# Kernel optimization log

Measured on AMD Instinct MI355X. Metric: run time of the kernel, lower is better.

The kernel has to match this reference:

```python
import jax, jax.numpy as jnp
import numpy as np

DIM = 1536
HEADS = 12
HD = DIM // HEADS  # 128
EPS = 1e-6
SINK_SIZE = 1          # frames
MAX_ATTN = 1920        # tokens (sliding window)


def setup_inputs() -> dict:
    key = jax.random.key(0)
    ks = jax.random.split(key, 10)
    B = 1
    F, H, W = 8, 16, 24
    L = F * H * W  # 3072
    s = 0.02
    inp = {
        "x": jax.random.normal(ks[0], (B, L, DIM), jnp.float32),
        "seq_lens": jnp.array([L], jnp.int32),
        "grid_sizes": jnp.array([[F, H, W]], jnp.int32),
        "freqs": jax.random.normal(ks[1], (1024, HD // 2, 2), jnp.float32),
        "wq": jax.random.normal(ks[2], (DIM, DIM), jnp.float32) * s,
        "bq": jnp.zeros((DIM,), jnp.float32),
        "wk": jax.random.normal(ks[3], (DIM, DIM), jnp.float32) * s,
        "bk": jnp.zeros((DIM,), jnp.float32),
        "wv": jax.random.normal(ks[4], (DIM, DIM), jnp.float32) * s,
        "bv": jnp.zeros((DIM,), jnp.float32),
        "wo": jax.random.normal(ks[5], (DIM, DIM), jnp.float32) * s,
        "bo": jnp.zeros((DIM,), jnp.float32),
        "nq_w": jnp.ones((DIM,), jnp.float32),
        "nk_w": jnp.ones((DIM,), jnp.float32),
    }
    return inp


def _rmsnorm(x, w):
    # WanRMSNorm: x * rsqrt(mean(x^2) + eps) * weight
    return x * jax.lax.rsqrt(jnp.mean(x * x, axis=-1, keepdims=True) + EPS) * w


def _rope(x, F, H, W, fc):
    # x: [B, L, n, d]; fc: complex [1024, d//2]
    B, L, n, d = x.shape
    c = d // 2
    c1 = c - 2 * (c // 3)  # temporal split
    c2 = c // 3
    f0, f1, f2 = fc[:, :c1], fc[:, c1:c1 + c2], fc[:, c1 + c2:]
    fr = jnp.concatenate([
        jnp.broadcast_to(f0[:F, None, None, :], (F, H, W, c1)),
        jnp.broadcast_to(f1[None, :H, None, :], (F, H, W, c2)),
        jnp.broadcast_to(f2[None, None, :W, :], (F, H, W, c2)),
    ], axis=-1).reshape(L, 1, c)  # [L, 1, c]
    xp = x.reshape(B, L, n, c, 2)
    xc = jax.lax.complex(xp[..., 0], xp[..., 1])  # [B, L, n, c]
    xr = xc * fr[None]
    return jnp.stack([jnp.real(xr), jnp.imag(xr)], axis=-1).reshape(B, L, n, d)


def reference(x, seq_lens, grid_sizes, freqs, wq, bq, wk, bk, wv, bv, wo, bo, nq_w, nk_w):
    B, L, _ = x.shape
    gs = np.asarray(grid_sizes)[0]
    F, H, W = int(gs[0]), int(gs[1]), int(gs[2])
    fs = H * W  # frame_seqlen
    sink = SINK_SIZE * fs

    q = _rmsnorm(x @ wq.T + bq, nq_w).reshape(B, L, HEADS, HD)
    k = _rmsnorm(x @ wk.T + bk, nk_w).reshape(B, L, HEADS, HD)
    v = (x @ wv.T + bv).reshape(B, L, HEADS, HD)

    fc = jax.lax.complex(freqs[..., 0], freqs[..., 1])  # [1024, HD//2]
    q = _rope(q, F, H, W, fc)
    k = _rope(k, F, H, W, fc)

    # sink + windowed frame-causal block mask (flex_attention block_mask)
    idx = jnp.arange(L)
    qf = idx // fs
    kf = idx // fs
    mask = (kf[None, :] <= qf[:, None]) & (
        (idx[None, :] < sink) | (idx[None, :] >= (qf[:, None] + 1) * fs - MAX_ATTN)
    )  # [L, L]

    scale = 1.0 / np.float32(np.sqrt(HD))
    scores = jnp.einsum('bqnd,bknd->bnqk', q, k) * scale
    scores = jnp.where(mask[None, None], scores, jnp.float32(-1e30))
    attn = jax.nn.softmax(scores, axis=-1)
    out = jnp.einsum('bnqk,bknd->bqnd', attn, v).reshape(B, L, DIM)
    return out @ wo.T + bo
```

## Files before the change

kernel.cpp:

```cpp
#include <hip/hip_runtime.h>
#include <stdint.h>

#define DIMC 1536
#define LTOK 3072
#define HEADS 12
#define HD 128
#define FS 384
#define MAXATTN 1920
#define HTOK 1152
#define NHT 1920

typedef __attribute__((ext_vector_type(4))) float f32x4;
typedef __attribute__((ext_vector_type(8))) short bf16x8;
typedef __attribute__((ext_vector_type(4))) unsigned int u32x4;

__device__ __forceinline__ unsigned short f2bf(float f) {
  union { float f; unsigned int u; } c; c.f = f;
  unsigned int u = c.u + 0x7fffu + ((c.u >> 16) & 1u);
  return (unsigned short)(u >> 16);
}
__device__ __forceinline__ float bf2f(unsigned short s) {
  union { unsigned int u; float f; } c; c.u = (unsigned int)s << 16; return c.f;
}

__device__ __forceinline__ void dma16(const void* g, void* l) {
  __builtin_amdgcn_global_load_lds(
      (const __attribute__((address_space(1))) unsigned int*)g,
      (__attribute__((address_space(3))) unsigned int*)l, 16, 0, 0);
}

__device__ __forceinline__ int vperm4(int G) {
  return (((G >> 3) & 1) << 3) | (((G >> 1) & 1) << 2) | ((G & 1) << 1) | ((G >> 2) & 1);
}

__global__ __launch_bounds__(256)
void cvt_all_k(const float* __restrict__ x, const float* __restrict__ wq,
               const float* __restrict__ wk, const float* __restrict__ wv,
               const float* __restrict__ wo,
               unsigned short* __restrict__ xb, unsigned short* __restrict__ wqb,
               unsigned short* __restrict__ wkb, unsigned short* __restrict__ wvb,
               unsigned short* __restrict__ wob)
{
  const int i = blockIdx.x * 256 + threadIdx.x;
  const int n0 = LTOK * DIMC / 4;
  const int nw = DIMC * DIMC / 4;
  const float* src; unsigned short* dst; int off;
  if (i < n0) { src = x; dst = xb; off = i; }
  else {
    int j = i - n0; int w = j / nw; off = j - w * nw;
    src = (w == 0) ? wq : (w == 1) ? wk : (w == 2) ? wv : wo;
    dst = (w == 0) ? wqb : (w == 1) ? wkb : (w == 2) ? wvb : wob;
  }
  float4 f = ((const float4*)src)[off];
  uint2 o;
  o.x = (unsigned int)f2bf(f.x) | ((unsigned int)f2bf(f.y) << 16);
  o.y = (unsigned int)f2bf(f.z) | ((unsigned int)f2bf(f.w) << 16);
  ((uint2*)dst)[off] = o;
}

__global__ __launch_bounds__(256)
void gemm_qkv(const unsigned short* __restrict__ A,
              const unsigned short* __restrict__ B0,
              const unsigned short* __restrict__ B1,
              const unsigned short* __restrict__ B2,
              const float* __restrict__ bias0,
              const float* __restrict__ bias1,
              const float* __restrict__ bias2,
              unsigned short* __restrict__ o0, unsigned short* __restrict__ o1,
              unsigned short* __restrict__ vt)
{
  const int z = blockIdx.z;
  const unsigned short* Bw = (z == 0) ? B0 : (z == 1) ? B1 : B2;
  const float* bias = (z == 0) ? bias0 : (z == 1) ? bias1 : bias2;

  __shared__ __align__(16) unsigned short lA[128 * 64];
  __shared__ __align__(16) unsigned short lB[128 * 64];

  const int tid = threadIdx.x;
  const int wave = tid >> 6;
  const int lane = tid & 63;
  const int m0 = blockIdx.y * 128;
  const int n0 = blockIdx.x * 128;
  const int wm = (wave >> 1) * 64;
  const int wn = (wave & 1) * 64;

  f32x4 acc[4][4] = {};

  const int srow = tid >> 3;
  const int scol = ((tid & 7) ^ (srow & 7)) * 8;
  const unsigned short* ga = A  + (size_t)(m0 + srow) * DIMC + scol;
  const unsigned short* gb = Bw + (size_t)(n0 + srow) * DIMC + scol;
  unsigned short* la = lA + tid * 8;
  unsigned short* lb = lB + tid * 8;

  const int fr = lane & 15;
  const int g = lane >> 4;
  const int fx = fr & 7;

  for (int k0 = 0; k0 < DIMC; k0 += 64) {
    dma16(ga + k0,                     la);
    dma16(ga + k0 + (size_t)32 * DIMC, la + 2048);
    dma16(ga + k0 + (size_t)64 * DIMC, la + 4096);
    dma16(ga + k0 + (size_t)96 * DIMC, la + 6144);
    dma16(gb + k0,                     lb);
    dma16(gb + k0 + (size_t)32 * DIMC, lb + 2048);
    dma16(gb + k0 + (size_t)64 * DIMC, lb + 4096);
    dma16(gb + k0 + (size_t)96 * DIMC, lb + 6144);
    __syncthreads();

#pragma unroll
    for (int kk = 0; kk < 2; ++kk) {
      const int cx = ((kk * 4 + g) ^ fx) * 8;
      bf16x8 af[4], bf[4];
#pragma unroll
      for (int i = 0; i < 4; ++i)
        af[i] = *(const bf16x8*)&lA[(wm + i * 16 + fr) * 64 + cx];
#pragma unroll
      for (int j = 0; j < 4; ++j)
        bf[j] = *(const bf16x8*)&lB[(wn + j * 16 + fr) * 64 + cx];
#pragma unroll
      for (int i = 0; i < 4; ++i)
#pragma unroll
        for (int j = 0; j < 4; ++j)
          acc[i][j] = __builtin_amdgcn_mfma_f32_16x16x32_bf16(af[i], bf[j], acc[i][j], 0, 0, 0);
    }
    __syncthreads();
  }

  const int col = lane & 15;
  const int rb = (lane >> 4) * 4;
  if (z < 2) {
    unsigned short* outp = z ? o1 : o0;
#pragma unroll
    for (int j = 0; j < 4; ++j) {
      const int gn = n0 + wn + j * 16 + col;
      const float bv = bias[gn];
#pragma unroll
      for (int i = 0; i < 4; ++i)
#pragma unroll
        for (int r = 0; r < 4; ++r) {
          const int gm = m0 + wm + i * 16 + rb + r;
          outp[(size_t)gm * DIMC + gn] = f2bf(acc[i][j][r] + bv);
        }
    }
  } else {
#pragma unroll
    for (int j = 0; j < 4; ++j) {
      const int gn = n0 + wn + j * 16 + col;
      const float bv = bias[gn];
#pragma unroll
      for (int i = 0; i < 4; ++i) {
        const int base = wm + i * 16 + rb;
        const int tile = base & ~63;
        const int toka = m0 + tile + vperm4((base & 63) >> 2) * 4;
        uint2 pk;
        pk.x = (unsigned int)f2bf(acc[i][j][0] + bv) |
               ((unsigned int)f2bf(acc[i][j][1] + bv) << 16);
        pk.y = (unsigned int)f2bf(acc[i][j][2] + bv) |
               ((unsigned int)f2bf(acc[i][j][3] + bv) << 16);
        *(uint2*)(vt + (size_t)gn * LTOK + toka) = pk;
      }
    }
  }
}

__global__ __launch_bounds__(256)
void gemm_wo(const unsigned short* __restrict__ A,
             const unsigned short* __restrict__ Bw,
             const float* __restrict__ bias,
             float* __restrict__ outp)
{
  __shared__ __align__(16) unsigned short lA[64 * 64];
  __shared__ __align__(16) unsigned short lB[128 * 64];

  const int tid = threadIdx.x;
  const int wave = tid >> 6;
  const int lane = tid & 63;
  const int m0 = blockIdx.y * 64;
  const int n0 = blockIdx.x * 128;
  const int wm = (wave >> 1) * 32;
  const int wn = (wave & 1) * 64;

  f32x4 acc[2][4] = {};

  const int srow = tid >> 3;
  const int scol = ((tid & 7) ^ (srow & 7)) * 8;
  const unsigned short* ga = A  + (size_t)(m0 + srow) * DIMC + scol;
  const unsigned short* gb = Bw + (size_t)(n0 + srow) * DIMC + scol;
  unsigned short* la = lA + tid * 8;
  unsigned short* lb = lB + tid * 8;

  const int fr = lane & 15;
  const int g = lane >> 4;
  const int fx = fr & 7;

  for (int k0 = 0; k0 < DIMC; k0 += 64) {
    dma16(ga + k0,                     la);
    dma16(ga + k0 + (size_t)32 * DIMC, la + 2048);
    dma16(gb + k0,                     lb);
    dma16(gb + k0 + (size_t)32 * DIMC, lb + 2048);
    dma16(gb + k0 + (size_t)64 * DIMC, lb + 4096);
    dma16(gb + k0 + (size_t)96 * DIMC, lb + 6144);
    __syncthreads();

#pragma unroll
    for (int kk = 0; kk < 2; ++kk) {
      const int cx = ((kk * 4 + g) ^ fx) * 8;
      bf16x8 af[2], bf[4];
#pragma unroll
      for (int i = 0; i < 2; ++i)
        af[i] = *(const bf16x8*)&lA[(wm + i * 16 + fr) * 64 + cx];
#pragma unroll
      for (int j = 0; j < 4; ++j)
        bf[j] = *(const bf16x8*)&lB[(wn + j * 16 + fr) * 64 + cx];
#pragma unroll
      for (int i = 0; i < 2; ++i)
#pragma unroll
        for (int j = 0; j < 4; ++j)
          acc[i][j] = __builtin_amdgcn_mfma_f32_16x16x32_bf16(af[i], bf[j], acc[i][j], 0, 0, 0);
    }
    __syncthreads();
  }

  const int col = lane & 15;
  const int rb = (lane >> 4) * 4;
#pragma unroll
  for (int j = 0; j < 4; ++j) {
    const int gn = n0 + wn + j * 16 + col;
    const float bv = bias[gn];
#pragma unroll
    for (int i = 0; i < 2; ++i)
#pragma unroll
      for (int r = 0; r < 4; ++r) {
        const int gm = m0 + wm + i * 16 + rb + r;
        outp[(size_t)gm * DIMC + gn] = acc[i][j][r] + bv;
      }
  }
}

__global__ __launch_bounds__(256)
void post_qkv_k(unsigned short* __restrict__ q, unsigned short* __restrict__ k,
                const float* __restrict__ nqw, const float* __restrict__ nkw,
                const float* __restrict__ freqs)
{
  const int bx = blockIdx.x;
  const int tid = threadIdx.x;
  const int which = bx >= LTOK;
  const int tok = bx - which * LTOK;
  unsigned short* row = (which ? k : q) + (size_t)tok * DIMC;
  const float* nw = which ? nkw : nqw;
  const float sc = which ? 1.f : (0.08838834764831845f * 1.4426950408889634f);
  const int base = tid * 6;

  float vv[6];
  float ss = 0.f;
#pragma unroll
  for (int j = 0; j < 6; ++j) {
    vv[j] = bf2f(row[base + j]);
    ss += vv[j] * vv[j];
  }
#pragma unroll
  for (int off = 1; off < 64; off <<= 1) ss += __shfl_xor(ss, off);
  __shared__ float wsum[4];
  if ((tid & 63) == 0) wsum[tid >> 6] = ss;
  __syncthreads();
  const float total = wsum[0] + wsum[1] + wsum[2] + wsum[3];
  const float rms = rsqrtf(total * (1.f / DIMC) + 1e-6f);

  const int f = tok / FS;
  const int rem = tok - f * FS;
  const int h = rem / 24;
  const int w = rem - h * 24;

#pragma unroll
  for (int pp = 0; pp < 3; ++pp) {
    const int P = (base >> 1) + pp;
    const int p = P & 63;
    const int t = (p < 22) ? f : ((p < 43) ? h : w);
    const float fre = freqs[t * 128 + p * 2];
    const float fim = freqs[t * 128 + p * 2 + 1];
    const float e = vv[2 * pp]     * rms * nw[base + 2 * pp];
    const float o = vv[2 * pp + 1] * rms * nw[base + 2 * pp + 1];
    row[base + 2 * pp]     = f2bf((e * fre - o * fim) * sc);
    row[base + 2 * pp + 1] = f2bf((e * fim + o * fre) * sc);
  }
}

#define KBUF (64 * 128)
#define VBUF (128 * 64)
__global__ __launch_bounds__(512, 4)
void attn_flash(const unsigned short* __restrict__ q,
                const unsigned short* __restrict__ k,
                const unsigned short* __restrict__ vt,
                unsigned short* __restrict__ ab,
                float* __restrict__ Opart,
                float* __restrict__ mlbuf)
{
  const int bid = blockIdx.x;
  int qb, head, chunk, nchunks;
  if (bid < 360) { const int hb = bid >> 1; qb = 23 - hb / 12; head = hb % 12; chunk = bid & 1; nchunks = 2; }
  else           { const int lb = bid - 360; qb = 8 - lb / 12; head = lb % 12; chunk = 0; nchunks = 1; }

  const int q0 = qb * 128;
  const int qf = qb / 3;
  const int kend = (qf + 1) * FS;
  const int s2 = kend - MAXATTN;
  const bool two = (s2 > FS);
  const int nt1 = (two ? FS : kend) >> 6;
  const int nt  = nt1 + (two ? (MAXATTN >> 6) : 0);
  const int half = nt / nchunks;
  const int tstart = chunk * half, tend = tstart + half;

  const int tid = threadIdx.x;
  const int wave = tid >> 6, lane = tid & 63;
  const int col = lane & 15;
  const int g = lane >> 4;
  const int g4 = g * 4;

  __shared__ __align__(16) unsigned short Kl[2 * KBUF];
  __shared__ __align__(16) unsigned short Vtl[2 * VBUF];

  bf16x8 qfA[4];
  {
    const unsigned short* qr0 = q + (size_t)(q0 + wave * 16 + col) * DIMC + head * HD;
#pragma unroll
    for (int kk = 0; kk < 4; ++kk)
      qfA[kk] = *(const bf16x8*)(qr0 + kk * 32 + g * 8);
  }

  f32x4 o0[8] = {};
  float m0 = -3.0e38f, l0 = 0.f;

  const int krow = tid >> 4;
  const int kc8  = ((tid & 15) ^ (krow & 15)) * 8;
  const unsigned short* kg = k + (size_t)krow * DIMC + head * HD + kc8;
  const int vrow = tid >> 3;
  const int vc8  = ((tid & 7) ^ (vrow & 7)) * 8;
  const unsigned short* vg = vt + ((size_t)head * HD + vrow) * LTOK + vc8;
  unsigned short* kl = Kl + tid * 8;
  unsigned short* vl = Vtl + tid * 8;

  {
    const int kb = (tstart < nt1) ? tstart * 64 : s2 + (tstart - nt1) * 64;
    const unsigned short* kp = kg + (size_t)kb * DIMC;
    dma16(kp,                     kl);
    dma16(kp + (size_t)32 * DIMC, kl + 32 * 128);
    const unsigned short* vp = vg + kb;
    dma16(vp,                     vl);
    dma16(vp + (size_t)64 * LTOK, vl + 64 * 64);
  }

  for (int t = tstart; t < tend; ++t) {
    const int kcur = ((t - tstart) & 1) * KBUF;
    const int vcur = ((t - tstart) & 1) * VBUF;
    __syncthreads();

    if (t + 1 < tend) {
      const int kb = (t + 1 < nt1) ? (t + 1) * 64 : s2 + (t + 1 - nt1) * 64;
      const int knxt = KBUF - kcur, vnxt = VBUF - vcur;
      const unsigned short* kp = kg + (size_t)kb * DIMC;
      dma16(kp,                     kl + knxt);
      dma16(kp + (size_t)32 * DIMC, kl + knxt + 32 * 128);
      const unsigned short* vp = vg + kb;
      dma16(vp,                     vl + vnxt);
      dma16(vp + (size_t)64 * LTOK, vl + vnxt + 64 * 64);
    }

    f32x4 sA[4] = {};
    __builtin_amdgcn_s_setprio(1);
#pragma unroll
    for (int kt = 0; kt < 4; ++kt) {
      const unsigned short* kr = &Kl[kcur + (kt * 16 + col) * 128];
#pragma unroll
      for (int kk = 0; kk < 4; ++kk) {
        bf16x8 kfr = *(const bf16x8*)(kr + ((kk * 4 + g) ^ col) * 8);
        sA[kt] = __builtin_amdgcn_mfma_f32_16x16x32_bf16(kfr, qfA[kk], sA[kt], 0, 0, 0);
      }
    }
    __builtin_amdgcn_s_setprio(0);

    unsigned int A0, A1, A2, A3, A4, A5, A6, A7;
    float alA;
    {
      float mx = sA[0][0];
#pragma unroll
      for (int kt = 0; kt < 4; ++kt)
#pragma unroll
        for (int r = 0; r < 4; ++r) mx = fmaxf(mx, sA[kt][r]);
      mx = fmaxf(mx, __shfl_xor(mx, 16));
      mx = fmaxf(mx, __shfl_xor(mx, 32));
      const float mn = fmaxf(m0, mx);
      alA = exp2f(m0 - mn);
      m0 = mn;
      float rs = 0.f;
#define PKA(KT, PA, PB)                                        \
      {                                                        \
        const unsigned short p0 = f2bf(exp2f(sA[KT][0] - mn)); \
        const unsigned short p1 = f2bf(exp2f(sA[KT][1] - mn)); \
        const unsigned short p2 = f2bf(exp2f(sA[KT][2] - mn)); \
        const unsigned short p3 = f2bf(exp2f(sA[KT][3] - mn)); \
        rs += bf2f(p0) + bf2f(p1) + bf2f(p2) + bf2f(p3);       \
        PA = (unsigned int)p0 | ((unsigned int)p1 << 16);      \
        PB = (unsigned int)p2 | ((unsigned int)p3 << 16);      \
      }
      PKA(0, A0, A1) PKA(1, A2, A3) PKA(2, A4, A5) PKA(3, A6, A7)
#undef PKA
      rs += __shfl_xor(rs, 16);
      rs += __shfl_xor(rs, 32);
      l0 = l0 * alA + rs;
    }

#pragma unroll
    for (int dt = 0; dt < 8; ++dt) o0[dt] *= alA;

    u32x4 tA0, tA1;
    tA0[0] = A0; tA0[1] = A1; tA0[2] = A2; tA0[3] = A3;
    tA1[0] = A4; tA1[1] = A5; tA1[2] = A6; tA1[3] = A7;
    const bf16x8 pfA0 = __builtin_bit_cast(bf16x8, tA0);
    const bf16x8 pfA1 = __builtin_bit_cast(bf16x8, tA1);

    const int vx0 = (g ^ (col & 7)) * 8;
    const int vx1 = ((4 + g) ^ (col & 7)) * 8;
    __builtin_amdgcn_s_setprio(1);
#pragma unroll
    for (int dt = 0; dt < 8; ++dt) {
      const unsigned short* vr = &Vtl[vcur + (dt * 16 + col) * 64];
      bf16x8 vf0 = *(const bf16x8*)(vr + vx0);
      o0[dt] = __builtin_amdgcn_mfma_f32_16x16x32_bf16(vf0, pfA0, o0[dt], 0, 0, 0);
      bf16x8 vf1 = *(const bf16x8*)(vr + vx1);
      o0[dt] = __builtin_amdgcn_mfma_f32_16x16x32_bf16(vf1, pfA1, o0[dt], 0, 0, 0);
    }
    __builtin_amdgcn_s_setprio(0);
  }

  const int qrow0 = q0 + wave * 16 + col;
  if (nchunks == 1) {
    const float i0 = 1.f / l0;
    unsigned short* or0 = ab + (size_t)qrow0 * DIMC + head * HD;
#pragma unroll
    for (int dt = 0; dt < 8; ++dt) {
      uint2 pk;
      pk.x = (unsigned int)f2bf(o0[dt][0] * i0) | ((unsigned int)f2bf(o0[dt][1] * i0) << 16);
      pk.y = (unsigned int)f2bf(o0[dt][2] * i0) | ((unsigned int)f2bf(o0[dt][3] * i0) << 16);
      *(uint2*)(or0 + dt * 16 + g4) = pk;
    }
  } else {
    const int tokp0 = qrow0 - HTOK;
    float* ob0 = Opart + ((size_t)(chunk * NHT + tokp0) * HEADS + head) * HD;
#pragma unroll
    for (int dt = 0; dt < 8; ++dt)
      *(f32x4*)(ob0 + dt * 16 + g4) = o0[dt];
    if (lane < 16) {
      float* mlp0 = mlbuf + 2 * ((size_t)(chunk * NHT + tokp0) * HEADS + head);
      mlp0[0] = m0; mlp0[1] = l0;
    }
  }
}

__global__ __launch_bounds__(384)
void merge_k(const float* __restrict__ Opart, const float* __restrict__ mlbuf,
             unsigned short* __restrict__ ab)
{
  const int tokp = blockIdx.x;
  const int tid = threadIdx.x;
  const int e = tid * 4;
  const int head = e >> 7;
  const size_t r0 = (size_t)tokp * DIMC + e;
  float4 o0 = *(const float4*)(Opart + r0);
  float4 o1 = *(const float4*)(Opart + (size_t)NHT * DIMC + r0);
  const float* ml0 = mlbuf + 2 * ((size_t)tokp * HEADS + head);
  const float* ml1 = mlbuf + 2 * ((size_t)(NHT + tokp) * HEADS + head);
  const float m0 = ml0[0], l0 = ml0[1], m1 = ml1[0], l1 = ml1[1];
  const float mm = fmaxf(m0, m1);
  const float a0 = exp2f(m0 - mm), a1 = exp2f(m1 - mm);
  const float inv = 1.f / (l0 * a0 + l1 * a1);
  uint2 pk;
  pk.x = (unsigned int)f2bf((o0.x * a0 + o1.x * a1) * inv) |
         ((unsigned int)f2bf((o0.y * a0 + o1.y * a1) * inv) << 16);
  pk.y = (unsigned int)f2bf((o0.z * a0 + o1.z * a1) * inv) |
         ((unsigned int)f2bf((o0.w * a0 + o1.w * a1) * inv) << 16);
  *(uint2*)(ab + (size_t)(HTOK + tokp) * DIMC + e) = pk;
}

extern "C" void kernel_launch(void* const* d_in, const int* in_sizes, int n_in,
                              void* d_out, int out_size, void* d_ws, size_t ws_size,
                              hipStream_t stream)
{
  (void)in_sizes; (void)n_in; (void)out_size; (void)ws_size;
  const float* x     = (const float*)d_in[0];
  const float* freqs = (const float*)d_in[3];
  const float* wq    = (const float*)d_in[4];
  const float* bq    = (const float*)d_in[5];
  const float* wk    = (const float*)d_in[6];
  const float* bk    = (const float*)d_in[7];
  const float* wv    = (const float*)d_in[8];
  const float* bv    = (const float*)d_in[9];
  const float* wo    = (const float*)d_in[10];
  const float* bo    = (const float*)d_in[11];
  const float* nqw   = (const float*)d_in[12];
  const float* nkw   = (const float*)d_in[13];

  char* ws = (char*)d_ws;
  size_t off = 0;
  auto take = [&](size_t bytes) -> void* {
    void* p = ws + off; off += (bytes + 255) & ~(size_t)255; return p;
  };
  unsigned short* wob = (unsigned short*)take((size_t)DIMC * DIMC * 2);
  unsigned short* qb  = (unsigned short*)take((size_t)LTOK * DIMC * 2);
  unsigned short* kb  = (unsigned short*)take((size_t)LTOK * DIMC * 2);
  unsigned short* vb  = (unsigned short*)take((size_t)LTOK * DIMC * 2);
  unsigned short* ab  = (unsigned short*)take((size_t)LTOK * DIMC * 2);
  unsigned short* vtb = (unsigned short*)take((size_t)LTOK * DIMC * 2);
  unsigned short* xb  = (unsigned short*)take((size_t)LTOK * DIMC * 2);
  unsigned short* wqb = (unsigned short*)take((size_t)DIMC * DIMC * 2);
  unsigned short* wkb = (unsigned short*)take((size_t)DIMC * DIMC * 2);
  unsigned short* wvb = (unsigned short*)take((size_t)DIMC * DIMC * 2);
  float* mlb = (float*)take((size_t)2 * NHT * HEADS * 2 * sizeof(float));
  float* Opart = (float*)xb;
  (void)vb;

  cvt_all_k<<<dim3(13824), dim3(256), 0, stream>>>(x, wq, wk, wv, wo,
                                                   xb, wqb, wkb, wvb, wob);

  gemm_qkv<<<dim3(DIMC / 128, LTOK / 128, 3), dim3(256), 0, stream>>>(
      xb, wqb, wkb, wvb, bq, bk, bv, qb, kb, vtb);

  post_qkv_k<<<dim3(2 * LTOK), dim3(256), 0, stream>>>(qb, kb, nqw, nkw, freqs);

  attn_flash<<<dim3(468), dim3(512), 0, stream>>>(qb, kb, vtb, ab, Opart, mlb);
  merge_k<<<dim3(NHT), dim3(384), 0, stream>>>(Opart, mlb, ab);

  gemm_wo<<<dim3(DIMC / 128, LTOK / 64), dim3(256), 0, stream>>>(
      ab, wob, bo, (float*)d_out);
}
```

Before: 281.9 us.

## Rebalance attention split-KV into three chunks and add lazy softmax rescaling

Reworks the attention block schedule so that query blocks with the longest key ranges (sink plus full window) are split into three KV chunks, and mid-length blocks into two. Heavy blocks are scheduled first, which aims to cut tail imbalance across CUs. A third partial buffer is written into the unused V workspace, and the merge kernel gains a third term. The online softmax now skips rescaling O and l unless the running max grows by more than 8 in log2 units, and it packs probabilities with v_cvt_pk_bf16_f32. The exchange is more partial traffic and merge work, plus probabilities that can reach 256 before normalisation.

```diff
diff --git a/kernel.cpp b/kernel.cpp
--- a/kernel.cpp
+++ b/kernel.cpp
@@ -21,6 +21,11 @@
 }
 __device__ __forceinline__ float bf2f(unsigned short s) {
   union { unsigned int u; float f; } c; c.u = (unsigned int)s << 16; return c.f;
+}
+__device__ __forceinline__ unsigned int cvtpk(float a, float b) {
+  unsigned int r;
+  asm("v_cvt_pk_bf16_f32 %0, %1, %2" : "=v"(r) : "v"(a), "v"(b));
+  return r;
 }
 
 __device__ __forceinline__ void dma16(const void* g, void* l) {
@@ -294,12 +299,17 @@
                 const unsigned short* __restrict__ vt,
                 unsigned short* __restrict__ ab,
                 float* __restrict__ Opart,
+                float* __restrict__ Opart2,
                 float* __restrict__ mlbuf)
 {
   const int bid = blockIdx.x;
-  int qb, head, chunk, nchunks;
-  if (bid < 360) { const int hb = bid >> 1; qb = 23 - hb / 12; head = hb % 12; chunk = bid & 1; nchunks = 2; }
-  else           { const int lb = bid - 360; qb = 8 - lb / 12; head = lb % 12; chunk = 0; nchunks = 1; }
+  int qb, head, chunk, nch;
+  if (bid < 36)       { qb = 6 + bid / 12; head = bid % 12; chunk = 0; nch = 1; }
+  else if (bid < 108) { int b = bid - 36;  qb = 12 + b / 24; int r = b % 24; head = r >> 1; chunk = r & 1; nch = 2; }
+  else if (bid < 432) { int b = bid - 108; qb = 15 + b / 36; int r = b % 36; head = r / 3; chunk = r % 3; nch = 3; }
+  else if (bid < 504) { int b = bid - 432; qb = 9 + b / 24;  int r = b % 24; head = r >> 1; chunk = r & 1; nch = 2; }
+  else if (bid < 540) { int b = bid - 504; qb = 3 + b / 12; head = b % 12; chunk = 0; nch = 1; }
+  else                { int b = bid - 540; qb = b / 12;     head = b % 12; chunk = 0; nch = 1; }
 
   const int q0 = qb * 128;
   const int qf = qb / 3;
@@ -308,7 +318,7 @@
   const bool two = (s2 > FS);
   const int nt1 = (two ? FS : kend) >> 6;
   const int nt  = nt1 + (two ? (MAXATTN >> 6) : 0);
-  const int half = nt / nchunks;
+  const int half = nt / nch;
   const int tstart = chunk * half, tend = tstart + half;
 
   const int tid = threadIdx.x;
@@ -379,43 +389,41 @@
     }
     __builtin_amdgcn_s_setprio(0);
 
-    unsigned int A0, A1, A2, A3, A4, A5, A6, A7;
-    float alA;
-    {
-      float mx = sA[0][0];
-#pragma unroll
-      for (int kt = 0; kt < 4; ++kt)
-#pragma unroll
-        for (int r = 0; r < 4; ++r) mx = fmaxf(mx, sA[kt][r]);
-      mx = fmaxf(mx, __shfl_xor(mx, 16));
-      mx = fmaxf(mx, __shfl_xor(mx, 32));
+    float mxa = fmaxf(fmaxf(sA[0][0], sA[0][1]), fmaxf(sA[0][2], sA[0][3]));
+    float mxb = fmaxf(fmaxf(sA[1][0], sA[1][1]), fmaxf(sA[1][2], sA[1][3]));
+    float mxc = fmaxf(fmaxf(sA[2][0], sA[2][1]), fmaxf(sA[2][2], sA[2][3]));
+    float mxd = fmaxf(fmaxf(sA[3][0], sA[3][1]), fmaxf(sA[3][2], sA[3][3]));
+    float mx = fmaxf(fmaxf(mxa, mxb), fmaxf(mxc, mxd));
+    mx = fmaxf(mx, __shfl_xor(mx, 16));
+    mx = fmaxf(mx, __shfl_xor(mx, 32));
+
+    if (!__all(mx <= m0 + 8.f)) {
       const float mn = fmaxf(m0, mx);
-      alA = exp2f(m0 - mn);
+      const float al = exp2f(m0 - mn);
       m0 = mn;
-      float rs = 0.f;
-#define PKA(KT, PA, PB)                                        \
-      {                                                        \
-        const unsigned short p0 = f2bf(exp2f(sA[KT][0] - mn)); \
-        const unsigned short p1 = f2bf(exp2f(sA[KT][1] - mn)); \
-        const unsigned short p2 = f2bf(exp2f(sA[KT][2] - mn)); \
-        const unsigned short p3 = f2bf(exp2f(sA[KT][3] - mn)); \
-        rs += bf2f(p0) + bf2f(p1) + bf2f(p2) + bf2f(p3);       \
-        PA = (unsigned int)p0 | ((unsigned int)p1 << 16);      \
-        PB = (unsigned int)p2 | ((unsigned int)p3 << 16);      \
-      }
-      PKA(0, A0, A1) PKA(1, A2, A3) PKA(2, A4, A5) PKA(3, A6, A7)
-#undef PKA
-      rs += __shfl_xor(rs, 16);
-      rs += __shfl_xor(rs, 32);
-      l0 = l0 * alA + rs;
-    }
-
-#pragma unroll
-    for (int dt = 0; dt < 8; ++dt) o0[dt] *= alA;
+      l0 *= al;
+#pragma unroll
+      for (int dt = 0; dt < 8; ++dt) o0[dt] *= al;
+    }
+
+    float p[16];
+#pragma unroll
+    for (int kt = 0; kt < 4; ++kt)
+#pragma unroll
+      for (int r = 0; r < 4; ++r)
+        p[kt * 4 + r] = exp2f(sA[kt][r] - m0);
+
+    float rs = ((p[0] + p[1]) + (p[2] + p[3])) + ((p[4] + p[5]) + (p[6] + p[7]))
+             + ((p[8] + p[9]) + (p[10] + p[11])) + ((p[12] + p[13]) + (p[14] + p[15]));
+    rs += __shfl_xor(rs, 16);
+    rs += __shfl_xor(rs, 32);
+    l0 += rs;
 
     u32x4 tA0, tA1;
-    tA0[0] = A0; tA0[1] = A1; tA0[2] = A2; tA0[3] = A3;
-    tA1[0] = A4; tA1[1] = A5; tA1[2] = A6; tA1[3] = A7;
+    tA0[0] = cvtpk(p[0], p[1]);   tA0[1] = cvtpk(p[2], p[3]);
+    tA0[2] = cvtpk(p[4], p[5]);   tA0[3] = cvtpk(p[6], p[7]);
+    tA1[0] = cvtpk(p[8], p[9]);   tA1[1] = cvtpk(p[10], p[11]);
+    tA1[2] = cvtpk(p[12], p[13]); tA1[3] = cvtpk(p[14], p[15]);
     const bf16x8 pfA0 = __builtin_bit_cast(bf16x8, tA0);
     const bf16x8 pfA1 = __builtin_bit_cast(bf16x8, tA1);
 
@@ -434,7 +442,7 @@
   }
 
   const int qrow0 = q0 + wave * 16 + col;
-  if (nchunks == 1) {
+  if (nch == 1) {
     const float i0 = 1.f / l0;
     unsigned short* or0 = ab + (size_t)qrow0 * DIMC + head * HD;
 #pragma unroll
@@ -446,7 +454,11 @@
     }
   } else {
     const int tokp0 = qrow0 - HTOK;
-    float* ob0 = Opart + ((size_t)(chunk * NHT + tokp0) * HEADS + head) * HD;
+    float* ob0;
+    if (chunk < 2)
+      ob0 = Opart + ((size_t)(chunk * NHT + tokp0) * HEADS + head) * HD;
+    else
+      ob0 = Opart2 + ((size_t)(tokp0 - 768) * HEADS + head) * HD;
 #pragma unroll
     for (int dt = 0; dt < 8; ++dt)
       *(f32x4*)(ob0 + dt * 16 + g4) = o0[dt];
@@ -458,8 +470,8 @@
 }
 
 __global__ __launch_bounds__(384)
-void merge_k(const float* __restrict__ Opart, const float* __restrict__ mlbuf,
-             unsigned short* __restrict__ ab)
+void merge_k(const float* __restrict__ Opart, const float* __restrict__ Opart2,
+             const float* __restrict__ mlbuf, unsigned short* __restrict__ ab)
 {
   const int tokp = blockIdx.x;
   const int tid = threadIdx.x;
@@ -471,14 +483,25 @@
   const float* ml0 = mlbuf + 2 * ((size_t)tokp * HEADS + head);
   const float* ml1 = mlbuf + 2 * ((size_t)(NHT + tokp) * HEADS + head);
   const float m0 = ml0[0], l0 = ml0[1], m1 = ml1[0], l1 = ml1[1];
-  const float mm = fmaxf(m0, m1);
+
+  const bool three = (tokp >= 768);
+  float m2 = -3.0e38f, l2 = 0.f;
+  float4 o2 = make_float4(0.f, 0.f, 0.f, 0.f);
+  if (three) {
+    o2 = *(const float4*)(Opart2 + (size_t)(tokp - 768) * DIMC + e);
+    const float* ml2 = mlbuf + 2 * ((size_t)(2 * NHT + tokp) * HEADS + head);
+    m2 = ml2[0]; l2 = ml2[1];
+  }
+
+  const float mm = fmaxf(fmaxf(m0, m1), m2);
   const float a0 = exp2f(m0 - mm), a1 = exp2f(m1 - mm);
-  const float inv = 1.f / (l0 * a0 + l1 * a1);
+  const float a2 = three ? exp2f(m2 - mm) : 0.f;
+  const float inv = 1.f / (l0 * a0 + l1 * a1 + l2 * a2);
   uint2 pk;
-  pk.x = (unsigned int)f2bf((o0.x * a0 + o1.x * a1) * inv) |
-         ((unsigned int)f2bf((o0.y * a0 + o1.y * a1) * inv) << 16);
-  pk.y = (unsigned int)f2bf((o0.z * a0 + o1.z * a1) * inv) |
-         ((unsigned int)f2bf((o0.w * a0 + o1.w * a1) * inv) << 16);
+  pk.x = (unsigned int)f2bf((o0.x * a0 + o1.x * a1 + o2.x * a2) * inv) |
+         ((unsigned int)f2bf((o0.y * a0 + o1.y * a1 + o2.y * a2) * inv) << 16);
+  pk.y = (unsigned int)f2bf((o0.z * a0 + o1.z * a1 + o2.z * a2) * inv) |
+         ((unsigned int)f2bf((o0.w * a0 + o1.w * a1 + o2.w * a2) * inv) << 16);
   *(uint2*)(ab + (size_t)(HTOK + tokp) * DIMC + e) = pk;
 }
 
@@ -515,9 +538,9 @@
   unsigned short* wqb = (unsigned short*)take((size_t)DIMC * DIMC * 2);
   unsigned short* wkb = (unsigned short*)take((size_t)DIMC * DIMC * 2);
   unsigned short* wvb = (unsigned short*)take((size_t)DIMC * DIMC * 2);
-  float* mlb = (float*)take((size_t)2 * NHT * HEADS * 2 * sizeof(float));
-  float* Opart = (float*)xb;
-  (void)vb;
+  float* mlb = (float*)take((size_t)3 * NHT * HEADS * 2 * sizeof(float));
+  float* Opart  = (float*)xb;
+  float* Opart2 = (float*)vb;
 
   cvt_all_k<<<dim3(13824), dim3(256), 0, stream>>>(x, wq, wk, wv, wo,
                                                    xb, wqb, wkb, wvb, wob);
@@ -527,8 +550,8 @@
 
   post_qkv_k<<<dim3(2 * LTOK), dim3(256), 0, stream>>>(qb, kb, nqw, nkw, freqs);
 
-  attn_flash<<<dim3(468), dim3(512), 0, stream>>>(qb, kb, vtb, ab, Opart, mlb);
-  merge_k<<<dim3(NHT), dim3(384), 0, stream>>>(Opart, mlb, ab);
+  attn_flash<<<dim3(576), dim3(512), 0, stream>>>(qb, kb, vtb, ab, Opart, Opart2, mlb);
+  merge_k<<<dim3(NHT), dim3(384), 0, stream>>>(Opart, Opart2, mlb, ab);
 
   gemm_wo<<<dim3(DIMC / 128, LTOK / 64), dim3(256), 0, stream>>>(
       ab, wob, bo, (float*)d_out);
```

Measured after the change: 278.4 us. No clear change (-1.2%).

## Process two key tiles per iteration with lazy rescale and rebalanced block split

Applied to the files above, without the earlier changes.

The attention loop now handles 128 keys per step as two 64-key tiles sharing one softmax update, with quad-buffered LDS staging. The online-softmax rescale of the output and row sum is skipped unless the running max grows by more than a threshold. The probability pack uses a hardware packed bf16 convert. Block-to-work assignment is rewritten into explicit groups with uneven chunk ranges to balance load. This trades halved occupancy (launch bound 2, doubled LDS) for fewer syncs and less softmax overhead per key. The grid size and tile counts are now hardcoded, so the loop assumes an even tile count in every range.

```diff
diff --git a/kernel.cpp b/kernel.cpp
--- a/kernel.cpp
+++ b/kernel.cpp
@@ -21,6 +21,11 @@
 }
 __device__ __forceinline__ float bf2f(unsigned short s) {
   union { unsigned int u; float f; } c; c.u = (unsigned int)s << 16; return c.f;
+}
+__device__ __forceinline__ unsigned int cvtpk(float a, float b) {
+  unsigned int r;
+  asm("v_cvt_pk_bf16_f32 %0, %1, %2" : "=v"(r) : "v"(a), "v"(b));
+  return r;
 }
 
 __device__ __forceinline__ void dma16(const void* g, void* l) {
@@ -288,7 +293,7 @@
 
 #define KBUF (64 * 128)
 #define VBUF (128 * 64)
-__global__ __launch_bounds__(512, 4)
+__global__ __launch_bounds__(512, 2)
 void attn_flash(const unsigned short* __restrict__ q,
                 const unsigned short* __restrict__ k,
                 const unsigned short* __restrict__ vt,
@@ -297,9 +302,13 @@
                 float* __restrict__ mlbuf)
 {
   const int bid = blockIdx.x;
-  int qb, head, chunk, nchunks;
-  if (bid < 360) { const int hb = bid >> 1; qb = 23 - hb / 12; head = hb % 12; chunk = bid & 1; nchunks = 2; }
-  else           { const int lb = bid - 360; qb = 8 - lb / 12; head = lb % 12; chunk = 0; nchunks = 1; }
+  int qb, head, chunk, nch, tstart, tend;
+  if (bid < 216)      { const int hb = bid >> 1; qb = 15 + hb / 12; head = hb % 12; chunk = bid & 1; nch = 2; tstart = chunk * 18; tend = tstart + 18; }
+  else if (bid < 252) { const int b = bid - 216; qb = 6 + b / 12; head = b % 12; chunk = 0; nch = 1; tstart = 0; tend = 18; }
+  else if (bid < 324) { const int b = bid - 252; const int hb = b >> 1; qb = 12 + hb / 12; head = hb % 12; chunk = b & 1; nch = 2; tstart = chunk ? 16 : 0; tend = chunk ? 30 : 16; }
+  else if (bid < 396) { const int b = bid - 324; const int hb = b >> 1; qb = 9 + hb / 12; head = hb % 12; chunk = b & 1; nch = 2; tstart = chunk * 12; tend = tstart + 12; }
+  else if (bid < 432) { const int b = bid - 396; qb = 3 + b / 12; head = b % 12; chunk = 0; nch = 1; tstart = 0; tend = 12; }
+  else                { const int b = bid - 432; qb = b / 12;     head = b % 12; chunk = 0; nch = 1; tstart = 0; tend = 6; }
 
   const int q0 = qb * 128;
   const int qf = qb / 3;
@@ -307,9 +316,6 @@
   const int s2 = kend - MAXATTN;
   const bool two = (s2 > FS);
   const int nt1 = (two ? FS : kend) >> 6;
-  const int nt  = nt1 + (two ? (MAXATTN >> 6) : 0);
-  const int half = nt / nchunks;
-  const int tstart = chunk * half, tend = tstart + half;
 
   const int tid = threadIdx.x;
   const int wave = tid >> 6, lane = tid & 63;
@@ -317,8 +323,8 @@
   const int g = lane >> 4;
   const int g4 = g * 4;
 
-  __shared__ __align__(16) unsigned short Kl[2 * KBUF];
-  __shared__ __align__(16) unsigned short Vtl[2 * VBUF];
+  __shared__ __align__(16) unsigned short Kl[4 * KBUF];
+  __shared__ __align__(16) unsigned short Vtl[4 * VBUF];
 
   bf16x8 qfA[4];
   {
@@ -337,104 +343,124 @@
   const int vrow = tid >> 3;
   const int vc8  = ((tid & 7) ^ (vrow & 7)) * 8;
   const unsigned short* vg = vt + ((size_t)head * HD + vrow) * LTOK + vc8;
-  unsigned short* kl = Kl + tid * 8;
-  unsigned short* vl = Vtl + tid * 8;
-
-  {
-    const int kb = (tstart < nt1) ? tstart * 64 : s2 + (tstart - nt1) * 64;
+
+  auto stage = [&](int t, int slot) {
+    const int kb = (t < nt1) ? t * 64 : s2 + (t - nt1) * 64;
     const unsigned short* kp = kg + (size_t)kb * DIMC;
+    unsigned short* kl = Kl + slot * KBUF + tid * 8;
     dma16(kp,                     kl);
     dma16(kp + (size_t)32 * DIMC, kl + 32 * 128);
     const unsigned short* vp = vg + kb;
+    unsigned short* vl = Vtl + slot * VBUF + tid * 8;
     dma16(vp,                     vl);
     dma16(vp + (size_t)64 * LTOK, vl + 64 * 64);
-  }
-
-  for (int t = tstart; t < tend; ++t) {
-    const int kcur = ((t - tstart) & 1) * KBUF;
-    const int vcur = ((t - tstart) & 1) * VBUF;
+  };
+
+  const int np = (tend - tstart) >> 1;
+  stage(tstart,     0);
+  stage(tstart + 1, 1);
+
+  for (int j = 0; j < np; ++j) {
+    const int cur = j & 1;
+    const int kbase = cur * (2 * KBUF);
+    const int vbase = cur * (2 * VBUF);
     __syncthreads();
 
-    if (t + 1 < tend) {
-      const int kb = (t + 1 < nt1) ? (t + 1) * 64 : s2 + (t + 1 - nt1) * 64;
-      const int knxt = KBUF - kcur, vnxt = VBUF - vcur;
-      const unsigned short* kp = kg + (size_t)kb * DIMC;
-      dma16(kp,                     kl + knxt);
-      dma16(kp + (size_t)32 * DIMC, kl + knxt + 32 * 128);
-      const unsigned short* vp = vg + kb;
-      dma16(vp,                     vl + vnxt);
-      dma16(vp + (size_t)64 * LTOK, vl + vnxt + 64 * 64);
-    }
-
-    f32x4 sA[4] = {};
+    if (j + 1 < np) {
+      const int tn = tstart + 2 * (j + 1);
+      stage(tn,     (cur ^ 1) * 2);
+      stage(tn + 1, (cur ^ 1) * 2 + 1);
+    }
+
+    f32x4 sA[4] = {}, sB[4] = {};
     __builtin_amdgcn_s_setprio(1);
 #pragma unroll
     for (int kt = 0; kt < 4; ++kt) {
-      const unsigned short* kr = &Kl[kcur + (kt * 16 + col) * 128];
+      const unsigned short* krA = &Kl[kbase + (kt * 16 + col) * 128];
 #pragma unroll
       for (int kk = 0; kk < 4; ++kk) {
-        bf16x8 kfr = *(const bf16x8*)(kr + ((kk * 4 + g) ^ col) * 8);
-        sA[kt] = __builtin_amdgcn_mfma_f32_16x16x32_bf16(kfr, qfA[kk], sA[kt], 0, 0, 0);
+        const int off = ((kk * 4 + g) ^ col) * 8;
+        bf16x8 ka = *(const bf16x8*)(krA + off);
+        bf16x8 kb2 = *(const bf16x8*)(krA + KBUF + off);
+        sA[kt] = __builtin_amdgcn_mfma_f32_16x16x32_bf16(ka,  qfA[kk], sA[kt], 0, 0, 0);
+        sB[kt] = __builtin_amdgcn_mfma_f32_16x16x32_bf16(kb2, qfA[kk], sB[kt], 0, 0, 0);
       }
     }
     __builtin_amdgcn_s_setprio(0);
 
-    unsigned int A0, A1, A2, A3, A4, A5, A6, A7;
-    float alA;
-    {
-      float mx = sA[0][0];
-#pragma unroll
-      for (int kt = 0; kt < 4; ++kt)
-#pragma unroll
-        for (int r = 0; r < 4; ++r) mx = fmaxf(mx, sA[kt][r]);
-      mx = fmaxf(mx, __shfl_xor(mx, 16));
-      mx = fmaxf(mx, __shfl_xor(mx, 32));
+    float a0 = fmaxf(fmaxf(sA[0][0], sA[0][1]), fmaxf(sA[0][2], sA[0][3]));
+    float a1 = fmaxf(fmaxf(sA[1][0], sA[1][1]), fmaxf(sA[1][2], sA[1][3]));
+    float a2 = fmaxf(fmaxf(sA[2][0], sA[2][1]), fmaxf(sA[2][2], sA[2][3]));
+    float a3 = fmaxf(fmaxf(sA[3][0], sA[3][1]), fmaxf(sA[3][2], sA[3][3]));
+    float b0 = fmaxf(fmaxf(sB[0][0], sB[0][1]), fmaxf(sB[0][2], sB[0][3]));
+    float b1 = fmaxf(fmaxf(sB[1][0], sB[1][1]), fmaxf(sB[1][2], sB[1][3]));
+    float b2 = fmaxf(fmaxf(sB[2][0], sB[2][1]), fmaxf(sB[2][2], sB[2][3]));
+    float b3 = fmaxf(fmaxf(sB[3][0], sB[3][1]), fmaxf(sB[3][2], sB[3][3]));
+    float mx = fmaxf(fmaxf(fmaxf(a0, a1), fmaxf(a2, a3)),
+                     fmaxf(fmaxf(b0, b1), fmaxf(b2, b3)));
+    mx = fmaxf(mx, __shfl_xor(mx, 16));
+    mx = fmaxf(mx, __shfl_xor(mx, 32));
+
+    if (!__all(mx <= m0 + 8.f)) {
       const float mn = fmaxf(m0, mx);
-      alA = exp2f(m0 - mn);
+      const float al = exp2f(m0 - mn);
       m0 = mn;
-      float rs = 0.f;
-#define PKA(KT, PA, PB)                                        \
-      {                                                        \
-        const unsigned short p0 = f2bf(exp2f(sA[KT][0] - mn)); \
-        const unsigned short p1 = f2bf(exp2f(sA[KT][1] - mn)); \
-        const unsigned short p2 = f2bf(exp2f(sA[KT][2] - mn)); \
-        const unsigned short p3 = f2bf(exp2f(sA[KT][3] - mn)); \
-        rs += bf2f(p0) + bf2f(p1) + bf2f(p2) + bf2f(p3);       \
-        PA = (unsigned int)p0 | ((unsigned int)p1 << 16);      \
-        PB = (unsigned int)p2 | ((unsigned int)p3 << 16);      \
+      l0 *= al;
+#pragma unroll
+      for (int dt = 0; dt < 8; ++dt) o0[dt] *= al;
+    }
+
+    float pa[16], pb[16];
+#pragma unroll
+    for (int kt = 0; kt < 4; ++kt)
+#pragma unroll
+      for (int r = 0; r < 4; ++r) {
+        pa[kt * 4 + r] = exp2f(sA[kt][r] - m0);
+        pb[kt * 4 + r] = exp2f(sB[kt][r] - m0);
       }
-      PKA(0, A0, A1) PKA(1, A2, A3) PKA(2, A4, A5) PKA(3, A6, A7)
-#undef PKA
-      rs += __shfl_xor(rs, 16);
-      rs += __shfl_xor(rs, 32);
-      l0 = l0 * alA + rs;
-    }
-
-#pragma unroll
-    for (int dt = 0; dt < 8; ++dt) o0[dt] *= alA;
-
-    u32x4 tA0, tA1;
-    tA0[0] = A0; tA0[1] = A1; tA0[2] = A2; tA0[3] = A3;
-    tA1[0] = A4; tA1[1] = A5; tA1[2] = A6; tA1[3] = A7;
+
+    float rs = (((pa[0] + pa[1]) + (pa[2] + pa[3])) + ((pa[4] + pa[5]) + (pa[6] + pa[7])))
+             + (((pa[8] + pa[9]) + (pa[10] + pa[11])) + ((pa[12] + pa[13]) + (pa[14] + pa[15])))
+             + (((pb[0] + pb[1]) + (pb[2] + pb[3])) + ((pb[4] + pb[5]) + (pb[6] + pb[7])))
+             + (((pb[8] + pb[9]) + (pb[10] + pb[11])) + ((pb[12] + pb[13]) + (pb[14] + pb[15])));
+    rs += __shfl_xor(rs, 16);
+    rs += __shfl_xor(rs, 32);
+    l0 += rs;
+
+    u32x4 tA0, tA1, tB0, tB1;
+    tA0[0] = cvtpk(pa[0], pa[1]);   tA0[1] = cvtpk(pa[2], pa[3]);
+    tA0[2] = cvtpk(pa[4], pa[5]);   tA0[3] = cvtpk(pa[6], pa[7]);
+    tA1[0] = cvtpk(pa[8], pa[9]);   tA1[1] = cvtpk(pa[10], pa[11]);
+    tA1[2] = cvtpk(pa[12], pa[13]); tA1[3] = cvtpk(pa[14], pa[15]);
+    tB0[0] = cvtpk(pb[0], pb[1]);   tB0[1] = cvtpk(pb[2], pb[3]);
+    tB0[2] = cvtpk(pb[4], pb[5]);   tB0[3] = cvtpk(pb[6], pb[7]);
+    tB1[0] = cvtpk(pb[8], pb[9]);   tB1[1] = cvtpk(pb[10], pb[11]);
+    tB1[2] = cvtpk(pb[12], pb[13]); tB1[3] = cvtpk(pb[14], pb[15]);
     const bf16x8 pfA0 = __builtin_bit_cast(bf16x8, tA0);
     const bf16x8 pfA1 = __builtin_bit_cast(bf16x8, tA1);
+    const bf16x8 pfB0 = __builtin_bit_cast(bf16x8, tB0);
+    const bf16x8 pfB1 = __builtin_bit_cast(bf16x8, tB1);
 
     const int vx0 = (g ^ (col & 7)) * 8;
     const int vx1 = ((4 + g) ^ (col & 7)) * 8;
     __builtin_amdgcn_s_setprio(1);
 #pragma unroll
     for (int dt = 0; dt < 8; ++dt) {
-      const unsigned short* vr = &Vtl[vcur + (dt * 16 + col) * 64];
-      bf16x8 vf0 = *(const bf16x8*)(vr + vx0);
-      o0[dt] = __builtin_amdgcn_mfma_f32_16x16x32_bf16(vf0, pfA0, o0[dt], 0, 0, 0);
-      bf16x8 vf1 = *(const bf16x8*)(vr + vx1);
-      o0[dt] = __builtin_amdgcn_mfma_f32_16x16x32_bf16(vf1, pfA1, o0[dt], 0, 0, 0);
+      const unsigned short* vrA = &Vtl[vbase + (dt * 16 + col) * 64];
+      bf16x8 v0 = *(const bf16x8*)(vrA + vx0);
+      o0[dt] = __builtin_amdgcn_mfma_f32_16x16x32_bf16(v0, pfA0, o0[dt], 0, 0, 0);
+      bf16x8 v1 = *(const bf16x8*)(vrA + vx1);
+      o0[dt] = __builtin_amdgcn_mfma_f32_16x16x32_bf16(v1, pfA1, o0[dt], 0, 0, 0);
+      bf16x8 v2 = *(const bf16x8*)(vrA + VBUF + vx0);
+      o0[dt] = __builtin_amdgcn_mfma_f32_16x16x32_bf16(v2, pfB0, o0[dt], 0, 0, 0);
+      bf16x8 v3 = *(const bf16x8*)(vrA + VBUF + vx1);
+      o0[dt] = __builtin_amdgcn_mfma_f32_16x16x32_bf16(v3, pfB1, o0[dt], 0, 0, 0);
     }
     __builtin_amdgcn_s_setprio(0);
   }
 
   const int qrow0 = q0 + wave * 16 + col;
-  if (nchunks == 1) {
+  if (nch == 1) {
     const float i0 = 1.f / l0;
     unsigned short* or0 = ab + (size_t)qrow0 * DIMC + head * HD;
 #pragma unroll
```

After: 281.8 us. No clear change (-0.1%).
